# Kernel optimization log

Hardware: AMD Instinct MI355X
Metric: run time of the kernel (lower is better)

## Reference

```python
import jax, jax.numpy as jnp
import numpy as np

N, T, F = 64, 256, 13          # nodes/frame, frames, node features
E = N * (N - 1)                 # complete directed graph (as in _extract_graph)
P, HID, HEADS = 128, 128, 4     # pooling_channels, hidden_dim, attention_heads


def setup_inputs() -> dict:
    key = jax.random.key(0)
    ks = jax.random.split(key, 32)
    s = 0.05
    src, dst = np.nonzero(~np.eye(N, dtype=bool))
    edge_index = jnp.array(np.stack([src, dst]), dtype=jnp.int32)
    C1 = P // HEADS
    rn = lambda k, shp: jax.random.normal(k, shp, jnp.float32) * s
    return {
        "x": jax.random.normal(ks[0], (T, N, F), jnp.float32),
        "edge_index": edge_index,
        "edge_attr": jax.random.uniform(ks[1], (T, E, 1), jnp.float32),
        # GATConv 1: in=F, heads=4, per-head C1, edge_dim=1, concat -> P
        "W1": rn(ks[2], (F, P)),
        "a_src1": rn(ks[3], (HEADS, C1)),
        "a_dst1": rn(ks[4], (HEADS, C1)),
        "We1": rn(ks[5], (1, P)),
        "a_edge1": rn(ks[6], (HEADS, C1)),
        "b1": jnp.zeros((P,), jnp.float32),
        # GATConv 2: in=P, heads=1, out=HID
        "W2": rn(ks[7], (P, HID)),
        "a_src2": rn(ks[8], (1, HID)),
        "a_dst2": rn(ks[9], (1, HID)),
        "We2": rn(ks[10], (1, HID)),
        "a_edge2": rn(ks[11], (1, HID)),
        "b2": jnp.zeros((HID,), jnp.float32),
        # AttentionalAggregation gate: Linear(HID, 1)
        "Wg": rn(ks[12], (HID, 1)),
        "bg": jnp.zeros((1,), jnp.float32),
        # bidirectional LSTM: input 2*HID, hidden HID (torch gate order i,f,g,o)
        "Wih_f": rn(ks[13], (4 * HID, 2 * HID)),
        "Whh_f": rn(ks[14], (4 * HID, HID)),
        "bih_f": jnp.zeros((4 * HID,), jnp.float32),
        "bhh_f": jnp.zeros((4 * HID,), jnp.float32),
        "Wih_b": rn(ks[15], (4 * HID, 2 * HID)),
        "Whh_b": rn(ks[16], (4 * HID, HID)),
        "bih_b": jnp.zeros((4 * HID,), jnp.float32),
        "bhh_b": jnp.zeros((4 * HID,), jnp.float32),
        # output layer: Linear(2*HID, 1)
        "Wo": rn(ks[17], (2 * HID, 1)),
        "bo": jnp.zeros((1,), jnp.float32),
    }


def reference(x, edge_index, edge_attr, W1, a_src1, a_dst1, We1, a_edge1, b1,
              W2, a_src2, a_dst2, We2, a_edge2, b2, Wg, bg,
              Wih_f, Whh_f, bih_f, bhh_f, Wih_b, Whh_b, bih_b, bhh_b, Wo, bo):
    n = x.shape[1]
    src, dst = edge_index[0], edge_index[1]

    def gat(h_in, ea, W, a_s, a_d, We, a_e, b):
        # PyG GATConv with edge_dim, add_self_loops=False, eval (no dropout)
        heads = a_s.shape[0]
        hc = W.shape[1]
        c = hc // heads
        h = (h_in @ W).reshape(-1, heads, c)          # [N, H, C]
        e = (ea @ We).reshape(-1, heads, c)           # [E, H, C]
        alpha = (h * a_s).sum(-1)[src] + (h * a_d).sum(-1)[dst] + (e * a_e).sum(-1)
        alpha = jax.nn.leaky_relu(alpha, 0.2)         # [E, H]
        amax = jax.ops.segment_max(alpha, dst, num_segments=n)
        amax = jnp.where(jnp.isfinite(amax), amax, 0.0)
        ex = jnp.exp(alpha - amax[dst])
        den = jax.ops.segment_sum(ex, dst, num_segments=n)
        coef = ex / (den[dst] + 1e-16)                # softmax per dst node
        out = jax.ops.segment_sum(h[src] * coef[:, :, None], dst, num_segments=n)
        return out.reshape(n, hc) + b

    def gnn(xt, eat):
        h1 = jax.nn.relu(gat(xt, eat, W1, a_src1, a_dst1, We1, a_edge1, b1))
        h2 = jax.nn.relu(gat(h1, eat, W2, a_src2, a_dst2, We2, a_edge2, b2))
        attn = jax.nn.softmax(h2 @ Wg + bg, axis=0)   # AttentionalAggregation
        return jnp.concatenate([(attn * h2).sum(0), h2.max(0)])  # [2*HID]

    embs = jax.vmap(gnn)(x, edge_attr)                # [T, 2*HID]

    def lstm(Wih, Whh, bih, bhh, seq):
        hid = Whh.shape[1]
        def step(carry, xt):
            h, c = carry
            g = xt @ Wih.T + h @ Whh.T + bih + bhh
            i, f, gg, o = jnp.split(g, 4)
            c = jax.nn.sigmoid(f) * c + jax.nn.sigmoid(i) * jnp.tanh(gg)
            h = jax.nn.sigmoid(o) * jnp.tanh(c)
            return (h, c), h
        init = (jnp.zeros((hid,), seq.dtype), jnp.zeros((hid,), seq.dtype))
        _, outs = jax.lax.scan(step, init, seq)
        return outs

    outs_f = lstm(Wih_f, Whh_f, bih_f, bhh_f, embs)
    outs_b = lstm(Wih_b, Whh_b, bih_b, bhh_b, embs[::-1])
    # lstm_out[:, -1, :] = [fwd state at t=T-1, bwd state at t=T-1]
    last = jnp.concatenate([outs_f[-1], outs_b[0]])
    return jax.nn.sigmoid(last @ Wo + bo)[None, :]    # [1, 1]
```

## Files before the change

kernel.cpp:

```cpp
#include <hip/hip_runtime.h>
#include <math.h>

#define NN 64
#define TT 256
#define FF 13
#define EE 4032
#define PP 128
#define HH 128

typedef float f32x4 __attribute__((ext_vector_type(4)));
typedef _Float16 f16x2 __attribute__((ext_vector_type(2)));

__device__ __forceinline__ float wave_max64(float v) {
#pragma unroll
  for (int off = 32; off > 0; off >>= 1) v = fmaxf(v, __shfl_xor(v, off, 64));
  return v;
}
__device__ __forceinline__ float wave_sum64(float v) {
#pragma unroll
  for (int off = 32; off > 0; off >>= 1) v += __shfl_xor(v, off, 64);
  return v;
}
__device__ __forceinline__ float sigm(float x) { return 1.f / (1.f + __expf(-x)); }
__device__ __forceinline__ float tanh_fast(float x) { return 1.f - 2.f / (__expf(2.f * x) + 1.f); }

__device__ __forceinline__ unsigned pk_f16(float lo, float hi) {
  unsigned u;
  asm("v_cvt_pkrtz_f16_f32 %0, %1, %2" : "=v"(u) : "v"(lo), "v"(hi));
  return u;
}

__device__ __forceinline__ float fdot2u(unsigned h, unsigned w, float acc) {
#if __has_builtin(__builtin_amdgcn_fdot2)
  return __builtin_amdgcn_fdot2(__builtin_bit_cast(f16x2, h),
                                __builtin_bit_cast(f16x2, w), acc, false);
#else
  const f16x2 a = __builtin_bit_cast(f16x2, h);
  const f16x2 b = __builtin_bit_cast(f16x2, w);
  return acc + (float)a.x * (float)b.x + (float)a.y * (float)b.y;
#endif
}

__device__ __forceinline__ float ror1(float x) {
  return __builtin_bit_cast(float, __builtin_amdgcn_mov_dpp(
      __builtin_bit_cast(int, x), 0x121, 0xF, 0xF, true));
}
__device__ __forceinline__ float qswap1(float x) {
  return __builtin_bit_cast(float, __builtin_amdgcn_mov_dpp(
      __builtin_bit_cast(int, x), 0xB1, 0xF, 0xF, true));
}

__global__ __launch_bounds__(512, 2)
void gnn_kernel(const float* __restrict__ x, const float* __restrict__ ea_g,
                const float* __restrict__ W1, const float* __restrict__ a_src1,
                const float* __restrict__ a_dst1, const float* __restrict__ We1,
                const float* __restrict__ a_edge1, const float* __restrict__ b1,
                const float* __restrict__ W2, const float* __restrict__ a_src2,
                const float* __restrict__ a_dst2, const float* __restrict__ We2,
                const float* __restrict__ a_edge2, const float* __restrict__ b2,
                const float* __restrict__ Wg, const float* __restrict__ bg,
                float* __restrict__ embs)
{
  __shared__ float x_s[NN * FF];
  __shared__ float W1_s[FF * PP];
  __shared__ float ea_s[EE];
  __shared__ float hA_s[NN * PP];
  __shared__ float hB_s[NN * PP];
  __shared__ float as1_s[NN * 4];
  __shared__ float ad1_s[NN * 4];
  __shared__ float asrc1_s[PP], adst1_s[PP], asrc2_s[PP], adst2_s[PP];
  __shared__ float b1_s[PP], b2_s[PP], Wg_s[PP];
  __shared__ float as2_s[NN], ad2_s[NN];
  __shared__ float coef_s[8 * 64 * 4];
  __shared__ float wed_s[8];
  __shared__ float attn_s[NN];

  const int tid = threadIdx.x;
  const int t = blockIdx.x;
  const int wave = tid >> 6, lane = tid & 63;

  for (int i = tid; i < NN * FF; i += 512) x_s[i] = x[t * NN * FF + i];
  for (int i = tid; i < FF * PP; i += 512) W1_s[i] = W1[i];
  for (int i = tid; i < EE; i += 512) ea_s[i] = ea_g[t * EE + i];
  if (tid < PP) {
    asrc1_s[tid] = a_src1[tid]; adst1_s[tid] = a_dst1[tid];
    asrc2_s[tid] = a_src2[tid]; adst2_s[tid] = a_dst2[tid];
    b1_s[tid] = b1[tid]; b2_s[tid] = b2[tid]; Wg_s[tid] = Wg[tid];
  }
  if (tid >= 128 && tid < 132) {
    const int h = tid - 128;
    float acc = 0.f;
    for (int c = 0; c < 32; ++c) acc += We1[h * 32 + c] * a_edge1[h * 32 + c];
    wed_s[h] = acc;
  }
  if (tid == 132) {
    float acc = 0.f;
    for (int c = 0; c < 128; ++c) acc += We2[c] * a_edge2[c];
    wed_s[4] = acc;
  }
  __syncthreads();

  {
    const int c = tid & 127, ib = tid >> 7;
    for (int q = 0; q < 16; ++q) {
      const int i = ib * 16 + q;
      float acc = 0.f;
#pragma unroll
      for (int f = 0; f < FF; ++f) acc += x_s[i * FF + f] * W1_s[f * PP + c];
      hA_s[i * PP + c] = acc;
    }
  }
  __syncthreads();

  {
    const int half = tid >> 8;
    const int tt2 = tid & 255;
    const int i = tt2 >> 2, h = tt2 & 3;
    const float* aw = half ? adst1_s : asrc1_s;
    float acc = 0.f;
    for (int cc = 0; cc < 32; ++cc) {
      const int c = (cc + tid) & 31;
      acc += hA_s[i * PP + h * 32 + c] * aw[h * 32 + c];
    }
    if (half) ad1_s[i * 4 + h] = acc; else as1_s[i * 4 + h] = acc;
  }
  __syncthreads();

  for (int kk = 0; kk < 8; ++kk) {
    const int d = kk * 8 + wave;
    {
      float a0, a1, a2, a3;
      if (lane < 63) {
        const int s = lane + (lane >= d ? 1 : 0);
        const int j = s * 63 + (d < s ? d : d - 1);
        const float ev = ea_s[j];
        a0 = as1_s[s * 4 + 0] + ad1_s[d * 4 + 0] + ev * wed_s[0];
        a1 = as1_s[s * 4 + 1] + ad1_s[d * 4 + 1] + ev * wed_s[1];
        a2 = as1_s[s * 4 + 2] + ad1_s[d * 4 + 2] + ev * wed_s[2];
        a3 = as1_s[s * 4 + 3] + ad1_s[d * 4 + 3] + ev * wed_s[3];
        a0 = a0 > 0.f ? a0 : 0.2f * a0;
        a1 = a1 > 0.f ? a1 : 0.2f * a1;
        a2 = a2 > 0.f ? a2 : 0.2f * a2;
        a3 = a3 > 0.f ? a3 : 0.2f * a3;
      } else { a0 = a1 = a2 = a3 = -1e30f; }
      const float m0 = wave_max64(a0), m1 = wave_max64(a1);
      const float m2 = wave_max64(a2), m3 = wave_max64(a3);
      const float p0 = (lane < 63) ? __expf(a0 - m0) : 0.f;
      const float p1 = (lane < 63) ? __expf(a1 - m1) : 0.f;
      const float p2 = (lane < 63) ? __expf(a2 - m2) : 0.f;
      const float p3 = (lane < 63) ? __expf(a3 - m3) : 0.f;
      const float s0 = wave_sum64(p0), s1 = wave_sum64(p1);
      const float s2 = wave_sum64(p2), s3 = wave_sum64(p3);
      float* cw = &coef_s[(wave * 64 + lane) * 4];
      cw[0] = p0 / (s0 + 1e-16f);
      cw[1] = p1 / (s1 + 1e-16f);
      cw[2] = p2 / (s2 + 1e-16f);
      cw[3] = p3 / (s3 + 1e-16f);
    }
    __syncthreads();
    {
      const int c0 = lane * 2;
      const int hh = c0 >> 5;
      float acc0 = 0.f, acc1 = 0.f;
      const float* cf = &coef_s[wave * 64 * 4 + hh];
      for (int s = 0; s < 63; ++s) {
        const int sn = s + (s >= d ? 1 : 0);
        const float cv = cf[s * 4];
        const float2 hv = *(const float2*)&hA_s[sn * PP + c0];
        acc0 += cv * hv.x; acc1 += cv * hv.y;
      }
      hB_s[d * PP + c0]     = fmaxf(acc0 + b1_s[c0], 0.f);
      hB_s[d * PP + c0 + 1] = fmaxf(acc1 + b1_s[c0 + 1], 0.f);
    }
    __syncthreads();
  }

  {
    const int c = tid & 127, ib = tid >> 7;
    float acc[16];
#pragma unroll
    for (int q = 0; q < 16; ++q) acc[q] = 0.f;
    for (int f0 = 0; f0 < 128; f0 += 4) {
      const float w0 = W2[(f0 + 0) * PP + c];
      const float w1 = W2[(f0 + 1) * PP + c];
      const float w2 = W2[(f0 + 2) * PP + c];
      const float w3 = W2[(f0 + 3) * PP + c];
#pragma unroll
      for (int q = 0; q < 16; ++q) {
        const float4 hv = *(const float4*)&hB_s[(ib * 16 + q) * PP + f0];
        acc[q] += hv.x * w0 + hv.y * w1 + hv.z * w2 + hv.w * w3;
      }
    }
#pragma unroll
    for (int q = 0; q < 16; ++q) hA_s[(ib * 16 + q) * PP + c] = acc[q];
  }
  __syncthreads();

  if (tid < 128) {
    const int i = tid >> 1, sel = tid & 1;
    const float* aw = sel ? adst2_s : asrc2_s;
    float acc = 0.f;
    for (int cc = 0; cc < 128; ++cc) {
      const int c = (cc + tid) & 127;
      acc += hA_s[i * PP + c] * aw[c];
    }
    if (sel) ad2_s[i] = acc; else as2_s[i] = acc;
  }
  __syncthreads();

  for (int kk = 0; kk < 8; ++kk) {
    const int d = kk * 8 + wave;
    {
      float a;
      if (lane < 63) {
        const int s = lane + (lane >= d ? 1 : 0);
        const int j = s * 63 + (d < s ? d : d - 1);
        a = as2_s[s] + ad2_s[d] + ea_s[j] * wed_s[4];
        a = a > 0.f ? a : 0.2f * a;
      } else a = -1e30f;
      const float m = wave_max64(a);
      const float p = (lane < 63) ? __expf(a - m) : 0.f;
      const float ssum = wave_sum64(p);
      coef_s[wave * 64 + lane] = p / (ssum + 1e-16f);
    }
    __syncthreads();
    {
      const int c0 = lane * 2;
      float acc0 = 0.f, acc1 = 0.f;
      const float* cf = &coef_s[wave * 64];
      for (int s = 0; s < 63; ++s) {
        const int sn = s + (s >= d ? 1 : 0);
        const float cv = cf[s];
        const float2 hv = *(const float2*)&hA_s[sn * PP + c0];
        acc0 += cv * hv.x; acc1 += cv * hv.y;
      }
      hB_s[d * PP + c0]     = fmaxf(acc0 + b2_s[c0], 0.f);
      hB_s[d * PP + c0 + 1] = fmaxf(acc1 + b2_s[c0 + 1], 0.f);
    }
    __syncthreads();
  }

  if (tid < 64) {
    float acc = 0.f;
    for (int cc = 0; cc < 128; ++cc) {
      const int c = (cc + tid) & 127;
      acc += hB_s[tid * PP + c] * Wg_s[c];
    }
    const float logit = acc + bg[0];
    const float m = wave_max64(logit);
    const float p = __expf(logit - m);
    const float ssum = wave_sum64(p);
    attn_s[tid] = p / ssum;
  }
  __syncthreads();
  if (tid < 128) {
    const int c = tid;
    float acc = 0.f, mx = -1e30f;
    for (int i = 0; i < NN; ++i) {
      const float v = hB_s[i * PP + c];
      acc += attn_s[i] * v;
      mx = fmaxf(mx, v);
    }
    embs[t * 256 + c] = acc;
    embs[t * 256 + 128 + c] = mx;
  }
}

__global__ __launch_bounds__(512, 2)
void zproj_kernel(const float* __restrict__ embs,
                  const float* __restrict__ Wih_f, const float* __restrict__ bih_f,
                  const float* __restrict__ bhh_f,
                  const float* __restrict__ Wih_b, const float* __restrict__ bih_b,
                  const float* __restrict__ bhh_b,
                  float* __restrict__ Z, float* __restrict__ Zb)
{
  __shared__ float e_s[256];
  const int t = blockIdx.x;
  const int j = threadIdx.x;
  const bool bwd = (t == TT);
  const int tsrc = bwd ? (TT - 1) : t;
  if (j < 256) e_s[j] = embs[tsrc * 256 + j];
  __syncthreads();
  const float* W = bwd ? Wih_b : Wih_f;
  float acc = bwd ? (bih_b[j] + bhh_b[j]) : (bih_f[j] + bhh_f[j]);
  const float4* Wr = (const float4*)(W + j * 256);
  const float4* er = (const float4*)e_s;
#pragma unroll 8
  for (int k = 0; k < 64; ++k) {
    const float4 w = Wr[k];
    const float4 e = er[k];
    acc += w.x * e.x + w.y * e.y + w.z * e.z + w.w * e.w;
  }
  if (bwd) Zb[j] = acc; else Z[t * 512 + j] = acc;
}

__global__ __launch_bounds__(1024)
void lstm_kernel(const float* __restrict__ Z, const float* __restrict__ Zb,
                 const float* __restrict__ Whh_f,
                 const float* __restrict__ Wo, const float* __restrict__ bo,
                 float* __restrict__ out)
{
  __shared__ float h_s[128];
  __shared__ __align__(16) unsigned h16_s[64];
  __shared__ float p_s[1024];
  __shared__ float hb_s[128];
  __shared__ float red_s[16];
  const int tid = threadIdx.x;
  const int j = tid & 511;
  const int s = tid >> 9;
  const int m = tid & 15;
  const int j0 = j & ~15;

  const float* wbase = Whh_f + s * 64 + 4 * m;
#define LWR(r) \
  unsigned wa##r, wb##r; { \
    const float4 v = *(const float4*)(wbase + (j0 + ((m - (r)) & 15)) * 128); \
    wa##r = pk_f16(v.x, v.y); wb##r = pk_f16(v.z, v.w); }
  LWR(0)  LWR(1)  LWR(2)  LWR(3)  LWR(4)  LWR(5)  LWR(6)  LWR(7)
  LWR(8)  LWR(9)  LWR(10) LWR(11) LWR(12) LWR(13) LWR(14) LWR(15)
#undef LWR
  asm volatile("" : "+v"(wa0),  "+v"(wb0),  "+v"(wa1),  "+v"(wb1),
                    "+v"(wa2),  "+v"(wb2),  "+v"(wa3),  "+v"(wb3),
                    "+v"(wa4),  "+v"(wb4),  "+v"(wa5),  "+v"(wb5),
                    "+v"(wa6),  "+v"(wb6),  "+v"(wa7),  "+v"(wb7));
  asm volatile("" : "+v"(wa8),  "+v"(wb8),  "+v"(wa9),  "+v"(wb9),
                    "+v"(wa10), "+v"(wb10), "+v"(wa11), "+v"(wb11),
                    "+v"(wa12), "+v"(wb12), "+v"(wa13), "+v"(wb13),
                    "+v"(wa14), "+v"(wb14), "+v"(wa15), "+v"(wb15));

  float c = 0.f;
  if (tid < 128) h_s[tid] = 0.f;
  if (tid < 64) h16_s[tid] = 0u;
  __syncthreads();

  float zcur = (s == 0) ? Z[j] : 0.f;
  for (int t = 0; t < TT; ++t) {
    const float znext = (s == 0 && t < TT - 1) ? Z[(t + 1) * 512 + j] : 0.f;
    const uint2 hd = *(const uint2*)&h16_s[s * 32 + 2 * m];
    float acc = 0.f;
#define STEP(r) \
    acc = fdot2u(hd.x, wa##r, acc); \
    acc = fdot2u(hd.y, wb##r, acc); \
    acc = ror1(acc);
    STEP(0)  STEP(1)  STEP(2)  STEP(3)  STEP(4)  STEP(5)  STEP(6)  STEP(7)
    STEP(8)  STEP(9)  STEP(10) STEP(11) STEP(12) STEP(13) STEP(14) STEP(15)
#undef STEP
    p_s[tid] = acc + zcur;
    __syncthreads();
    if (tid < 128) {
      const float gi = p_s[tid]       + p_s[512 + tid];
      const float gf = p_s[128 + tid] + p_s[640 + tid];
      const float gg = p_s[256 + tid] + p_s[768 + tid];
      const float go = p_s[384 + tid] + p_s[896 + tid];
      c = sigm(gf) * c + sigm(gi) * tanh_fast(gg);
      const float hnew = sigm(go) * tanh_fast(c);
      h_s[tid] = hnew;
      const float hnb = qswap1(hnew);
      if (!(tid & 1)) h16_s[tid >> 1] = pk_f16(hnew, hnb);
    }
    __syncthreads();
    zcur = znext;
  }

  if (tid < 128) {
    const float gi = Zb[tid], gg = Zb[256 + tid], go = Zb[384 + tid];
    const float cb = sigm(gi) * tanh_fast(gg);
    hb_s[tid] = sigm(go) * tanh_fast(cb);
  }
  __syncthreads();

  float v = 0.f;
  if (tid < 128) v = h_s[tid] * Wo[tid];
  else if (tid < 256) v = hb_s[tid - 128] * Wo[tid];
  v = wave_sum64(v);
  if ((tid & 63) == 0) red_s[tid >> 6] = v;
  __syncthreads();
  if (tid == 0) {
    float sum = bo[0];
#pragma unroll
    for (int k = 0; k < 16; ++k) sum += red_s[k];
    out[0] = 1.f / (1.f + __expf(-sum));
  }
}

extern "C" void kernel_launch(void* const* d_in, const int* in_sizes, int n_in,
                              void* d_out, int out_size, void* d_ws, size_t ws_size,
                              hipStream_t stream) {
  const float* x       = (const float*)d_in[0];
  const float* ea      = (const float*)d_in[2];
  const float* W1      = (const float*)d_in[3];
  const float* a_src1  = (const float*)d_in[4];
  const float* a_dst1  = (const float*)d_in[5];
  const float* We1     = (const float*)d_in[6];
  const float* a_edge1 = (const float*)d_in[7];
  const float* b1      = (const float*)d_in[8];
  const float* W2      = (const float*)d_in[9];
  const float* a_src2  = (const float*)d_in[10];
  const float* a_dst2  = (const float*)d_in[11];
  const float* We2     = (const float*)d_in[12];
  const float* a_edge2 = (const float*)d_in[13];
  const float* b2      = (const float*)d_in[14];
  const float* Wg      = (const float*)d_in[15];
  const float* bg      = (const float*)d_in[16];
  const float* Wih_f   = (const float*)d_in[17];
  const float* Whh_f   = (const float*)d_in[18];
  const float* bih_f   = (const float*)d_in[19];
  const float* bhh_f   = (const float*)d_in[20];
  const float* Wih_b   = (const float*)d_in[21];
  const float* bih_b   = (const float*)d_in[23];
  const float* bhh_b   = (const float*)d_in[24];
  const float* Wo      = (const float*)d_in[25];
  const float* bo      = (const float*)d_in[26];
  float* out = (float*)d_out;

  float* embs = (float*)d_ws;
  float* Z    = embs + 256 * 256;
  float* Zb   = Z + 256 * 512;

  gnn_kernel<<<256, 512, 0, stream>>>(x, ea, W1, a_src1, a_dst1, We1, a_edge1, b1,
                                      W2, a_src2, a_dst2, We2, a_edge2, b2, Wg, bg, embs);
  zproj_kernel<<<257, 512, 0, stream>>>(embs, Wih_f, bih_f, bhh_f, Wih_b, bih_b, bhh_b, Z, Zb);
  lstm_kernel<<<1, 1024, 0, stream>>>(Z, Zb, Whh_f, Wo, bo, out);
}
```

Measured before the change: 282.4 us.

## Restructure GNN attention aggregation with batched destinations, DPP reductions, and register-tiled GEMM

Wave reductions now use DPP row rotations plus readlane instead of shfl_xor, which avoids LDS-based cross-lane traffic. The attention coefficients for 16 destinations are computed before each barrier rather than 8, and the self-loop is handled by zeroing its coefficient so the aggregation loop runs over all 64 sources without per-step index fixups. Aggregation moves to float4 vectorised loads, with normalisation deferred to a single multiply by the inverse denominator. The W2 projection becomes a 4x4 register tile per thread with float4 weight loads. The cost is more shared memory for the coefficient buffers and more register pressure.

```diff
diff --git a/kernel.cpp b/kernel.cpp
--- a/kernel.cpp
+++ b/kernel.cpp
@@ -11,11 +11,6 @@
 typedef float f32x4 __attribute__((ext_vector_type(4)));
 typedef _Float16 f16x2 __attribute__((ext_vector_type(2)));
 
-__device__ __forceinline__ float wave_max64(float v) {
-#pragma unroll
-  for (int off = 32; off > 0; off >>= 1) v = fmaxf(v, __shfl_xor(v, off, 64));
-  return v;
-}
 __device__ __forceinline__ float wave_sum64(float v) {
 #pragma unroll
   for (int off = 32; off > 0; off >>= 1) v += __shfl_xor(v, off, 64);
@@ -23,13 +18,28 @@
 }
 __device__ __forceinline__ float sigm(float x) { return 1.f / (1.f + __expf(-x)); }
 __device__ __forceinline__ float tanh_fast(float x) { return 1.f - 2.f / (__expf(2.f * x) + 1.f); }
+
+#define ROTF(x, N) __builtin_bit_cast(float, __builtin_amdgcn_mov_dpp( \
+    __builtin_bit_cast(int, x), 0x120 + (N), 0xF, 0xF, true))
+__device__ __forceinline__ float rdlane(float v, int l) {
+  return __builtin_bit_cast(float, __builtin_amdgcn_readlane(__builtin_bit_cast(int, v), l));
+}
+__device__ __forceinline__ float allred_max(float v) {
+  v = fmaxf(v, ROTF(v, 1)); v = fmaxf(v, ROTF(v, 2));
+  v = fmaxf(v, ROTF(v, 4)); v = fmaxf(v, ROTF(v, 8));
+  return fmaxf(fmaxf(rdlane(v, 0), rdlane(v, 16)),
+               fmaxf(rdlane(v, 32), rdlane(v, 48)));
+}
+__device__ __forceinline__ float allred_sum(float v) {
+  v += ROTF(v, 1); v += ROTF(v, 2); v += ROTF(v, 4); v += ROTF(v, 8);
+  return (rdlane(v, 0) + rdlane(v, 16)) + (rdlane(v, 32) + rdlane(v, 48));
+}
 
 __device__ __forceinline__ unsigned pk_f16(float lo, float hi) {
   unsigned u;
   asm("v_cvt_pkrtz_f16_f32 %0, %1, %2" : "=v"(u) : "v"(lo), "v"(hi));
   return u;
 }
-
 __device__ __forceinline__ float fdot2u(unsigned h, unsigned w, float acc) {
 #if __has_builtin(__builtin_amdgcn_fdot2)
   return __builtin_amdgcn_fdot2(__builtin_bit_cast(f16x2, h),
@@ -40,7 +50,6 @@
   return acc + (float)a.x * (float)b.x + (float)a.y * (float)b.y;
 #endif
 }
-
 __device__ __forceinline__ float ror1(float x) {
   return __builtin_bit_cast(float, __builtin_amdgcn_mov_dpp(
       __builtin_bit_cast(int, x), 0x121, 0xF, 0xF, true));
@@ -66,12 +75,15 @@
   __shared__ float ea_s[EE];
   __shared__ float hA_s[NN * PP];
   __shared__ float hB_s[NN * PP];
-  __shared__ float as1_s[NN * 4];
-  __shared__ float ad1_s[NN * 4];
+  __shared__ float as1_s[4 * NN];
+  __shared__ float ad1_s[4 * NN];
   __shared__ float asrc1_s[PP], adst1_s[PP], asrc2_s[PP], adst2_s[PP];
   __shared__ float b1_s[PP], b2_s[PP], Wg_s[PP];
   __shared__ float as2_s[NN], ad2_s[NN];
-  __shared__ float coef_s[8 * 64 * 4];
+  __shared__ __align__(16) float coefA_s[16 * 272];
+  __shared__ float denA_s[16 * 4];
+  __shared__ __align__(16) float coefB_s[16 * 68];
+  __shared__ float denB_s[16];
   __shared__ float wed_s[8];
   __shared__ float attn_s[NN];
 
@@ -122,77 +134,105 @@
       const int c = (cc + tid) & 31;
       acc += hA_s[i * PP + h * 32 + c] * aw[h * 32 + c];
     }
-    if (half) ad1_s[i * 4 + h] = acc; else as1_s[i * 4 + h] = acc;
-  }
-  __syncthreads();
-
-  for (int kk = 0; kk < 8; ++kk) {
-    const int d = kk * 8 + wave;
-    {
+    if (half) ad1_s[h * 64 + i] = acc; else as1_s[h * 64 + i] = acc;
+  }
+  __syncthreads();
+
+  for (int g = 0; g < 4; ++g) {
+#pragma unroll
+    for (int r = 0; r < 2; ++r) {
+      const int d = g * 16 + r * 8 + wave;
+      const int dl = d & 15;
       float a0, a1, a2, a3;
-      if (lane < 63) {
-        const int s = lane + (lane >= d ? 1 : 0);
-        const int j = s * 63 + (d < s ? d : d - 1);
-        const float ev = ea_s[j];
-        a0 = as1_s[s * 4 + 0] + ad1_s[d * 4 + 0] + ev * wed_s[0];
-        a1 = as1_s[s * 4 + 1] + ad1_s[d * 4 + 1] + ev * wed_s[1];
-        a2 = as1_s[s * 4 + 2] + ad1_s[d * 4 + 2] + ev * wed_s[2];
-        a3 = as1_s[s * 4 + 3] + ad1_s[d * 4 + 3] + ev * wed_s[3];
+      if (lane != d) {
+        const int jj = lane * 63 + (d < lane ? d : d - 1);
+        const float ev = ea_s[jj];
+        a0 = as1_s[0 * 64 + lane] + ad1_s[0 * 64 + d] + ev * wed_s[0];
+        a1 = as1_s[1 * 64 + lane] + ad1_s[1 * 64 + d] + ev * wed_s[1];
+        a2 = as1_s[2 * 64 + lane] + ad1_s[2 * 64 + d] + ev * wed_s[2];
+        a3 = as1_s[3 * 64 + lane] + ad1_s[3 * 64 + d] + ev * wed_s[3];
         a0 = a0 > 0.f ? a0 : 0.2f * a0;
         a1 = a1 > 0.f ? a1 : 0.2f * a1;
         a2 = a2 > 0.f ? a2 : 0.2f * a2;
         a3 = a3 > 0.f ? a3 : 0.2f * a3;
       } else { a0 = a1 = a2 = a3 = -1e30f; }
-      const float m0 = wave_max64(a0), m1 = wave_max64(a1);
-      const float m2 = wave_max64(a2), m3 = wave_max64(a3);
-      const float p0 = (lane < 63) ? __expf(a0 - m0) : 0.f;
-      const float p1 = (lane < 63) ? __expf(a1 - m1) : 0.f;
-      const float p2 = (lane < 63) ? __expf(a2 - m2) : 0.f;
-      const float p3 = (lane < 63) ? __expf(a3 - m3) : 0.f;
-      const float s0 = wave_sum64(p0), s1 = wave_sum64(p1);
-      const float s2 = wave_sum64(p2), s3 = wave_sum64(p3);
-      float* cw = &coef_s[(wave * 64 + lane) * 4];
-      cw[0] = p0 / (s0 + 1e-16f);
-      cw[1] = p1 / (s1 + 1e-16f);
-      cw[2] = p2 / (s2 + 1e-16f);
-      cw[3] = p3 / (s3 + 1e-16f);
+      const float m0 = allred_max(a0), m1 = allred_max(a1);
+      const float m2 = allred_max(a2), m3 = allred_max(a3);
+      const float p0 = (lane != d) ? __expf(a0 - m0) : 0.f;
+      const float p1 = (lane != d) ? __expf(a1 - m1) : 0.f;
+      const float p2 = (lane != d) ? __expf(a2 - m2) : 0.f;
+      const float p3 = (lane != d) ? __expf(a3 - m3) : 0.f;
+      const float s0 = allred_sum(p0), s1 = allred_sum(p1);
+      const float s2 = allred_sum(p2), s3 = allred_sum(p3);
+      coefA_s[dl * 272 + 0 * 68 + lane] = p0;
+      coefA_s[dl * 272 + 1 * 68 + lane] = p1;
+      coefA_s[dl * 272 + 2 * 68 + lane] = p2;
+      coefA_s[dl * 272 + 3 * 68 + lane] = p3;
+      if (lane == 0) {
+        denA_s[dl * 4 + 0] = s0; denA_s[dl * 4 + 1] = s1;
+        denA_s[dl * 4 + 2] = s2; denA_s[dl * 4 + 3] = s3;
+      }
     }
     __syncthreads();
     {
-      const int c0 = lane * 2;
+      const int half = lane >> 5;
+      const int dl = wave * 2 + half;
+      const int d  = g * 16 + dl;
+      const int c0 = (lane & 31) * 4;
       const int hh = c0 >> 5;
-      float acc0 = 0.f, acc1 = 0.f;
-      const float* cf = &coef_s[wave * 64 * 4 + hh];
-      for (int s = 0; s < 63; ++s) {
-        const int sn = s + (s >= d ? 1 : 0);
-        const float cv = cf[s * 4];
-        const float2 hv = *(const float2*)&hA_s[sn * PP + c0];
-        acc0 += cv * hv.x; acc1 += cv * hv.y;
+      const float* cfb = &coefA_s[dl * 272 + hh * 68];
+      float ac0 = 0.f, ac1 = 0.f, ac2 = 0.f, ac3 = 0.f;
+#pragma unroll 4
+      for (int s = 0; s < 64; s += 4) {
+        const float4 cf = *(const float4*)&cfb[s];
+        const float4 h0 = *(const float4*)&hA_s[(s + 0) * PP + c0];
+        ac0 += cf.x * h0.x; ac1 += cf.x * h0.y; ac2 += cf.x * h0.z; ac3 += cf.x * h0.w;
+        const float4 h1v = *(const float4*)&hA_s[(s + 1) * PP + c0];
+        ac0 += cf.y * h1v.x; ac1 += cf.y * h1v.y; ac2 += cf.y * h1v.z; ac3 += cf.y * h1v.w;
+        const float4 h2v = *(const float4*)&hA_s[(s + 2) * PP + c0];
+        ac0 += cf.z * h2v.x; ac1 += cf.z * h2v.y; ac2 += cf.z * h2v.z; ac3 += cf.z * h2v.w;
+        const float4 h3v = *(const float4*)&hA_s[(s + 3) * PP + c0];
+        ac0 += cf.w * h3v.x; ac1 += cf.w * h3v.y; ac2 += cf.w * h3v.z; ac3 += cf.w * h3v.w;
       }
-      hB_s[d * PP + c0]     = fmaxf(acc0 + b1_s[c0], 0.f);
-      hB_s[d * PP + c0 + 1] = fmaxf(acc1 + b1_s[c0 + 1], 0.f);
+      const float inv = 1.f / (denA_s[dl * 4 + hh] + 1e-16f);
+      const float4 bv = *(const float4*)&b1_s[c0];
+      float4 o;
+      o.x = fmaxf(ac0 * inv + bv.x, 0.f);
+      o.y = fmaxf(ac1 * inv + bv.y, 0.f);
+      o.z = fmaxf(ac2 * inv + bv.z, 0.f);
+      o.w = fmaxf(ac3 * inv + bv.w, 0.f);
+      *(float4*)&hB_s[d * PP + c0] = o;
     }
     __syncthreads();
   }
 
   {
-    const int c = tid & 127, ib = tid >> 7;
-    float acc[16];
-#pragma unroll
-    for (int q = 0; q < 16; ++q) acc[q] = 0.f;
+    const int cg = tid & 31, ig = tid >> 5;
+    const int c0 = cg * 4, i0 = ig * 4;
+    float acc[4][4];
+#pragma unroll
+    for (int ii = 0; ii < 4; ++ii)
+#pragma unroll
+      for (int cc = 0; cc < 4; ++cc) acc[ii][cc] = 0.f;
     for (int f0 = 0; f0 < 128; f0 += 4) {
-      const float w0 = W2[(f0 + 0) * PP + c];
-      const float w1 = W2[(f0 + 1) * PP + c];
-      const float w2 = W2[(f0 + 2) * PP + c];
-      const float w3 = W2[(f0 + 3) * PP + c];
-#pragma unroll
-      for (int q = 0; q < 16; ++q) {
-        const float4 hv = *(const float4*)&hB_s[(ib * 16 + q) * PP + f0];
-        acc[q] += hv.x * w0 + hv.y * w1 + hv.z * w2 + hv.w * w3;
+      float4 wv0 = *(const float4*)&W2[(f0 + 0) * PP + c0];
+      float4 wv1 = *(const float4*)&W2[(f0 + 1) * PP + c0];
+      float4 wv2 = *(const float4*)&W2[(f0 + 2) * PP + c0];
+      float4 wv3 = *(const float4*)&W2[(f0 + 3) * PP + c0];
+#pragma unroll
+      for (int ii = 0; ii < 4; ++ii) {
+        const float4 hv = *(const float4*)&hB_s[(i0 + ii) * PP + f0];
+        acc[ii][0] += hv.x * wv0.x + hv.y * wv1.x + hv.z * wv2.x + hv.w * wv3.x;
+        acc[ii][1] += hv.x * wv0.y + hv.y * wv1.y + hv.z * wv2.y + hv.w * wv3.y;
+        acc[ii][2] += hv.x * wv0.z + hv.y * wv1.z + hv.z * wv2.z + hv.w * wv3.z;
+        acc[ii][3] += hv.x * wv0.w + hv.y * wv1.w + hv.z * wv2.w + hv.w * wv3.w;
       }
     }
 #pragma unroll
-    for (int q = 0; q < 16; ++q) hA_s[(ib * 16 + q) * PP + c] = acc[q];
+    for (int ii = 0; ii < 4; ++ii) {
+      float4 o; o.x = acc[ii][0]; o.y = acc[ii][1]; o.z = acc[ii][2]; o.w = acc[ii][3];
+      *(float4*)&hA_s[(i0 + ii) * PP + c0] = o;
+    }
   }
   __syncthreads();
 
@@ -208,34 +248,51 @@
   }
   __syncthreads();
 
-  for (int kk = 0; kk < 8; ++kk) {
-    const int d = kk * 8 + wave;
-    {
+  for (int g = 0; g < 4; ++g) {
+#pragma unroll
+    for (int r = 0; r < 2; ++r) {
+      const int d = g * 16 + r * 8 + wave;
+      const int dl = d & 15;
       float a;
-      if (lane < 63) {
-        const int s = lane + (lane >= d ? 1 : 0);
-        const int j = s * 63 + (d < s ? d : d - 1);
-        a = as2_s[s] + ad2_s[d] + ea_s[j] * wed_s[4];
+      if (lane != d) {
+        const int jj = lane * 63 + (d < lane ? d : d - 1);
+        a = as2_s[lane] + ad2_s[d] + ea_s[jj] * wed_s[4];
         a = a > 0.f ? a : 0.2f * a;
       } else a = -1e30f;
-      const float m = wave_max64(a);
-      const float p = (lane < 63) ? __expf(a - m) : 0.f;
-      const float ssum = wave_sum64(p);
-      coef_s[wave * 64 + lane] = p / (ssum + 1e-16f);
+      const float m = allred_max(a);
+      const float p = (lane != d) ? __expf(a - m) : 0.f;
+      const float ssum = allred_sum(p);
+      coefB_s[dl * 68 + lane] = p;
+      if (lane == 0) denB_s[dl] = ssum;
     }
     __syncthreads();
     {
-      const int c0 = lane * 2;
-      float acc0 = 0.f, acc1 = 0.f;
-      const float* cf = &coef_s[wave * 64];
-      for (int s = 0; s < 63; ++s) {
-        const int sn = s + (s >= d ? 1 : 0);
-        const float cv = cf[s];
-        const float2 hv = *(const float2*)&hA_s[sn * PP + c0];
-        acc0 += cv * hv.x; acc1 += cv * hv.y;
+      const int half = lane >> 5;
+      const int dl = wave * 2 + half;
+      const int d  = g * 16 + dl;
+      const int c0 = (lane & 31) * 4;
+      const float* cfb = &coefB_s[dl * 68];
+      float ac0 = 0.f, ac1 = 0.f, ac2 = 0.f, ac3 = 0.f;
+#pragma unroll 4
+      for (int s = 0; s < 64; s += 4) {
+        const float4 cf = *(const float4*)&cfb[s];
+        const float4 h0 = *(const float4*)&hA_s[(s + 0) * PP + c0];
+        ac0 += cf.x * h0.x; ac1 += cf.x * h0.y; ac2 += cf.x * h0.z; ac3 += cf.x * h0.w;
+        const float4 h1v = *(const float4*)&hA_s[(s + 1) * PP + c0];
+        ac0 += cf.y * h1v.x; ac1 += cf.y * h1v.y; ac2 += cf.y * h1v.z; ac3 += cf.y * h1v.w;
+        const float4 h2v = *(const float4*)&hA_s[(s + 2) * PP + c0];
+        ac0 += cf.z * h2v.x; ac1 += cf.z * h2v.y; ac2 += cf.z * h2v.z; ac3 += cf.z * h2v.w;
+        const float4 h3v = *(const float4*)&hA_s[(s + 3) * PP + c0];
+        ac0 += cf.w * h3v.x; ac1 += cf.w * h3v.y; ac2 += cf.w * h3v.z; ac3 += cf.w * h3v.w;
       }
-      hB_s[d * PP + c0]     = fmaxf(acc0 + b2_s[c0], 0.f);
-      hB_s[d * PP + c0 + 1] = fmaxf(acc1 + b2_s[c0 + 1], 0.f);
+      const float inv = 1.f / (denB_s[dl] + 1e-16f);
+      const float4 bv = *(const float4*)&b2_s[c0];
+      float4 o;
+      o.x = fmaxf(ac0 * inv + bv.x, 0.f);
+      o.y = fmaxf(ac1 * inv + bv.y, 0.f);
+      o.z = fmaxf(ac2 * inv + bv.z, 0.f);
+      o.w = fmaxf(ac3 * inv + bv.w, 0.f);
+      *(float4*)&hB_s[d * PP + c0] = o;
     }
     __syncthreads();
   }
@@ -247,9 +304,9 @@
       acc += hB_s[tid * PP + c] * Wg_s[c];
     }
     const float logit = acc + bg[0];
-    const float m = wave_max64(logit);
+    const float m = allred_max(logit);
     const float p = __expf(logit - m);
-    const float ssum = wave_sum64(p);
+    const float ssum = allred_sum(p);
     attn_s[tid] = p / ssum;
   }
   __syncthreads();
```

After: 260.4 us. 1.08x faster.
